# Optimization experiments

Hardware: AMD Instinct MI355X
Metric: run time of the kernel (lower is better)

## Reference

```python
import jax, jax.numpy as jnp
import numpy as np

B, L, D, H, HD, K = 1, 1024, 1024, 16, 64, 16
EPS = 1e-5

def _l2norm(x):
    n = jnp.sqrt(jnp.sum(x * x, axis=-1, keepdims=True))
    return x / jnp.maximum(n, 1e-12)

def _lin(x, w, b):
    return x @ w.T + b

def _lrelu2(x, alpha=0.01):
    y = jnp.where(x > 0, x, alpha * x)
    return y * y

def _forward(x, spectral_basis, M_phi_w, M_phi_b, wq_w, wq_b, wk_w, wk_b,
             wv_w, wv_b, wo_w, wo_b, wg_z_w, wg_z_b, kv_norm_scale):
    Bx, Lx, Dx = x.shape
    bhld = x.reshape(Bx, Lx, H, HD).transpose(0, 2, 1, 3)          # [B,H,L,h]
    # stu_conv: causal conv of every channel with each of K shared filters (FFT form)
    n = 2 * Lx
    Xf = jnp.fft.rfft(bhld, n=n, axis=2)                            # [B,H,F,h]
    Ff = jnp.fft.rfft(spectral_basis, n=n, axis=0)                  # [F,K]
    conv = jnp.fft.irfft(Xf[:, :, :, None, :] * Ff[None, None, :, :, None], n=n, axis=2)[:, :, :Lx]  # [B,H,L,K,h]
    x_tilde = conv.transpose(0, 2, 3, 1, 4).reshape(Bx, Lx, K * H * HD)
    x_tilde = _lin(x_tilde, M_phi_w, M_phi_b)                       # [B,L,D]
    q = _lin(x_tilde, wq_w, wq_b).reshape(Bx, Lx, H, HD).transpose(0, 2, 1, 3)
    k = _lin(x_tilde, wk_w, wk_b).reshape(Bx, Lx, H, HD).transpose(0, 2, 1, 3)
    v = _lin(x_tilde, wv_w, wv_b).reshape(Bx, Lx, H, HD).transpose(0, 2, 1, 3)
    k = _l2norm(k)
    v = _l2norm(v)
    sim = jnp.einsum('bhld,bhld->bhl', q, k)                        # [B,H,L]
    # Z[b,h,s,p,n] = k[b,h,s,n] * v[b,h,s,p]
    Z = v[..., :, None] * k[..., None, :]                           # [B,H,L,h,h]
    Z = Z * kv_norm_scale
    gates_logits = Z.reshape(Bx, H, Lx, HD * HD) @ wg_z_w.T + wg_z_b  # [B,H,L,1]
    gates_z = (_lrelu2(gates_logits) + EPS)[..., 0]                 # [B,H,L]
    gated_Z = Z * gates_z[..., None, None]
    # online-softmax associative scan over sequence: running (max, norm, exp-weighted v)
    def combine(a, b):
        ma, na, va = a
        mb, nb, vb = b
        m = jnp.maximum(ma, mb)
        ea = jnp.exp(ma - m)
        eb = jnp.exp(mb - m)
        return (m, na * ea + nb * eb, va * ea[..., None] + vb * eb[..., None])
    max_cumul, norm_cumul, v_cumul = jax.lax.associative_scan(
        combine, (sim, jnp.ones_like(sim), v), axis=2)
    Z_cumul = jnp.cumsum(gated_Z, axis=2)
    gate_cumul = jnp.cumsum(gates_z, axis=2)
    linear_attn = v_cumul / (norm_cumul[..., None] + EPS)           # [B,H,L,h]
    weights = jnp.exp(sim - max_cumul) / (norm_cumul + EPS)         # [B,H,L]
    Hm = Z_cumul / (gate_cumul[..., None, None] + EPS)              # [B,H,L,h,h]
    Y_base = jnp.einsum('bhtp,bhtpn->bhtn', q, Hm)                  # [B,H,L,h]
    # torch einsum broadcasts the size-1 p-dim of linear_attn.unsqueeze(-2):
    Y_lin = jnp.sum(q, axis=-1, keepdims=True) * linear_attn        # [B,H,L,h]
    Y = Y_base + (Y_lin - Y_base) * weights[..., None]
    Y = Y.transpose(0, 2, 1, 3).reshape(Bx, Lx, Dx)
    Y = _l2norm(Y)
    return _lin(Y, wo_w, wo_b)

def setup_inputs() -> dict:
    key = jax.random.key(0)
    ks = jax.random.split(key, 16)
    def nrm(k, shape, scale):
        return jax.random.normal(k, shape, dtype=jnp.float32) * scale
    return {
        'x': nrm(ks[0], (B, L, D), 1.0),
        'spectral_basis': nrm(ks[1], (L, K), 1.0 / np.sqrt(L)),
        'M_phi_w': nrm(ks[2], (D, K * H * HD), 1.0 / np.sqrt(K * H * HD)),
        'M_phi_b': jnp.zeros((D,), jnp.float32),
        'wq_w': nrm(ks[3], (D, D), 1.0 / np.sqrt(D)),
        'wq_b': jnp.zeros((D,), jnp.float32),
        'wk_w': nrm(ks[4], (D, D), 1.0 / np.sqrt(D)),
        'wk_b': jnp.zeros((D,), jnp.float32),
        'wv_w': nrm(ks[5], (D, D), 1.0 / np.sqrt(D)),
        'wv_b': jnp.zeros((D,), jnp.float32),
        'wo_w': nrm(ks[6], (D, D), 1.0 / np.sqrt(D)),
        'wo_b': jnp.zeros((D,), jnp.float32),
        'wg_z_w': nrm(ks[7], (1, HD * HD), 1.0 / np.sqrt(HD * HD)),
        'wg_z_b': jnp.zeros((1,), jnp.float32),
        'kv_norm_scale': jnp.ones((1, H, 1, 1, 1), jnp.float32),
    }

def reference(x, spectral_basis, M_phi_w, M_phi_b, wq_w, wq_b, wk_w, wk_b,
              wv_w, wv_b, wo_w, wo_b, wg_z_w, wg_z_b, kv_norm_scale):
    return _forward(x, spectral_basis, M_phi_w, M_phi_b, wq_w, wq_b, wk_w, wk_b,
                    wv_w, wv_b, wo_w, wo_b, wg_z_w, wg_z_b, kv_norm_scale)
```

## Files before the change

kernel.cpp:

```cpp
#include <hip/hip_runtime.h>
#include <hip/hip_bf16.h>

typedef __hip_bfloat16 bf16;
typedef __attribute__((ext_vector_type(8))) short short8;
typedef __attribute__((ext_vector_type(4))) float f32x4;

struct bf16x8 { bf16 v[8]; };
struct bf16x4 { bf16 v[4]; };

__device__ __forceinline__ void gload_lds16(const void* g, void* l) {
  __builtin_amdgcn_global_load_lds(
      (const __attribute__((address_space(1))) void*)g,
      (__attribute__((address_space(3))) void*)l, 16, 0, 0);
}

__device__ __forceinline__ float wave_sum(float x) {
#pragma unroll
  for (int o = 32; o > 0; o >>= 1) x += __shfl_xor(x, o, 64);
  return x;
}

__global__ void prep_cast_k(const float* __restrict__ mphiW,
                            const float* __restrict__ wq, const float* __restrict__ wk,
                            const float* __restrict__ wv, const float* __restrict__ wo,
                            const float* __restrict__ x,
                            const float* __restrict__ bq, const float* __restrict__ bk,
                            const float* __restrict__ bv,
                            bf16* __restrict__ mphi_bf, bf16* __restrict__ wqkv,
                            bf16* __restrict__ wo_bf, bf16* __restrict__ x_bf,
                            float* __restrict__ qkv_bias) {
  int b = blockIdx.x, tid = threadIdx.x;
  const float* src; bf16* dst; int i;
  if (b < 8192) { src = mphiW; dst = mphi_bf; i = b * 256 + tid; }
  else if (b < 10240) {
    int bb = b - 8192;
    src = (bb < 512) ? wq : (bb < 1024) ? wk : (bb < 1536) ? wv : wo;
    dst = (bb < 512) ? wqkv : (bb < 1024) ? (wqkv + 1048576)
         : (bb < 1536) ? (wqkv + 2097152) : wo_bf;
    i = (bb & 511) * 256 + tid;
  } else if (b < 10752) { src = x; dst = x_bf; i = (b - 10240) * 256 + tid; }
  else {
    int j = (b - 10752) * 256 + tid;
    if (j < 3072) {
      const float* s = (j < 1024) ? bq : (j < 2048) ? bk : bv;
      qkv_bias[j] = s[j & 1023];
    }
    return;
  }
  const float4* p = (const float4*)src + (size_t)i * 2;
  float4 a = p[0], c = p[1];
  bf16x8 o;
  o.v[0] = __float2bfloat16(a.x); o.v[1] = __float2bfloat16(a.y);
  o.v[2] = __float2bfloat16(a.z); o.v[3] = __float2bfloat16(a.w);
  o.v[4] = __float2bfloat16(c.x); o.v[5] = __float2bfloat16(c.y);
  o.v[6] = __float2bfloat16(c.z); o.v[7] = __float2bfloat16(c.w);
  ((bf16x8*)dst)[i] = o;
}

__global__ void build_T_k(const float* __restrict__ basis, bf16* __restrict__ T) {
  size_t i8 = (size_t)blockIdx.x * 256 + threadIdx.x;
  size_t i = i8 * 8;
  int s0 = (int)(i & 1023);
  int l = (int)((i >> 10) & 1023);
  int k = (int)(i >> 20);
  bf16x8 o;
#pragma unroll
  for (int j = 0; j < 8; j++) {
    int s = s0 + j;
    o.v[j] = (s <= l) ? __float2bfloat16(basis[(size_t)(l - s) * 16 + k])
                      : __float2bfloat16(0.f);
  }
  ((bf16x8*)T)[i8] = o;
}

template<int TRI, int OUTBF, int HASB, int DBUF>
__global__ void gemm_bt(const bf16* __restrict__ A, long sAb, int lda,
                        const bf16* __restrict__ B, long sBb, int ldb,
                        void* __restrict__ Cv, void* __restrict__ Cv2, int nbz1,
                        long sCb, int ldc,
                        const float* __restrict__ bias, int sbias, int K) {
  constexpr int NB = DBUF ? 2 : 1;
  __shared__ bf16 As[NB][128 * 64];
  __shared__ bf16 Bs[NB][128 * 64];
  const int tid = threadIdx.x;
  const int lane = tid & 63;
  const int wid = tid >> 6;
  const int wr = wid >> 1, wc = wid & 1;
  const int cpx = gridDim.x >> 3;
  const int logical = (blockIdx.x & 7) * cpx + (blockIdx.x >> 3);
  const int bx = logical & 7, by = (logical >> 3) & 7, bz = logical >> 6;
  const int r0 = by * 128, c0 = bx * 128;
  const bf16* Ab = A + (size_t)bz * sAb;
  const bf16* Bb = B + (size_t)bz * sBb;
  f32x4 acc[4][4] = {};
  const int nt = (TRI ? min(K, r0 + 128) : K) >> 6;

  const int srow = tid >> 3, scol = (tid & 7) << 3;

#define STAGE(buf, t)                                                         \
  {                                                                           \
    const int k0_ = (t) << 6;                                                 \
    _Pragma("unroll")                                                         \
    for (int i = 0; i < 4; i++) {                                             \
      int row = i * 32 + srow;                                                \
      gload_lds16(Ab + (size_t)(r0 + row) * lda + k0_ + scol,                 \
                  &As[buf][(row << 6) + scol]);                               \
    }                                                                         \
    _Pragma("unroll")                                                         \
    for (int i = 0; i < 4; i++) {                                             \
      int row = i * 32 + srow;                                                \
      gload_lds16(Bb + (size_t)(c0 + row) * ldb + k0_ + scol,                 \
                  &Bs[buf][(row << 6) + scol]);                               \
    }                                                                         \
  }

  int cur = 0;
  if (DBUF) STAGE(0, 0)
  for (int t = 0; t < nt; ++t) {
    if (DBUF) {
      if (t + 1 < nt) {
        STAGE(cur ^ 1, t + 1)
        asm volatile("s_waitcnt vmcnt(8)" ::: "memory");
      } else {
        asm volatile("s_waitcnt vmcnt(0)" ::: "memory");
      }
      __syncthreads();
    } else {
      __syncthreads();
      STAGE(0, t)
      asm volatile("s_waitcnt vmcnt(0)" ::: "memory");
      __syncthreads();
    }
#pragma unroll
    for (int ks = 0; ks < 2; ks++) {
      const int colo = ks * 32 + (lane >> 4) * 8;
      short8 af[4], bfr[4];
#pragma unroll
      for (int m = 0; m < 4; m++)
        af[m] = *(const short8*)&As[cur][(wr * 64 + m * 16 + (lane & 15)) * 64 + colo];
#pragma unroll
      for (int n = 0; n < 4; n++)
        bfr[n] = *(const short8*)&Bs[cur][(wc * 64 + n * 16 + (lane & 15)) * 64 + colo];
#pragma unroll
      for (int m = 0; m < 4; m++)
#pragma unroll
        for (int n = 0; n < 4; n++)
          acc[m][n] = __builtin_amdgcn_mfma_f32_16x16x32_bf16(af[m], bfr[n], acc[m][n], 0, 0, 0);
    }
    if (DBUF) { __syncthreads(); cur ^= 1; }
  }
#undef STAGE

  void* Cb = (bz < nbz1) ? Cv : Cv2;
  const int bzl = (bz < nbz1) ? bz : bz - nbz1;
  const int rb = r0 + wr * 64 + ((lane >> 4) << 2);
  const int cb = c0 + wc * 64 + (lane & 15);
#pragma unroll
  for (int n = 0; n < 4; n++) {
    const int col = cb + n * 16;
    float bv = HASB ? bias[bz * sbias + col] : 0.f;
#pragma unroll
    for (int m = 0; m < 4; m++) {
#pragma unroll
      for (int j = 0; j < 4; j++) {
        const int row = rb + m * 16 + j;
        size_t off = (size_t)bzl * sCb + (size_t)row * ldc + col;
        float v = acc[m][n][j] + bv;
        if (OUTBF) ((bf16*)Cb)[off] = __float2bfloat16(v);
        else       ((float*)Cb)[off] = v;
      }
    }
  }
}

__global__ void reduce16_k(const float* __restrict__ pA, const float* __restrict__ pB,
                           const float* __restrict__ bias, bf16* __restrict__ out) {
  int i4 = blockIdx.x * 256 + threadIdx.x;
  float4 v = *((const float4*)bias + (i4 & 255));
#pragma unroll
  for (int j = 0; j < 8; j++) {
    float4 a = *((const float4*)pA + i4 + j * 262144);
    v.x += a.x; v.y += a.y; v.z += a.z; v.w += a.w;
  }
#pragma unroll
  for (int j = 0; j < 8; j++) {
    float4 a = *((const float4*)pB + i4 + j * 262144);
    v.x += a.x; v.y += a.y; v.z += a.z; v.w += a.w;
  }
  bf16x4 o;
  o.v[0] = __float2bfloat16(v.x); o.v[1] = __float2bfloat16(v.y);
  o.v[2] = __float2bfloat16(v.z); o.v[3] = __float2bfloat16(v.w);
  ((bf16x4*)out)[i4] = o;
}

__global__ void reduce4f_k(const float* __restrict__ p, const float* __restrict__ bias,
                           float* __restrict__ out) {
  int i4 = blockIdx.x * 256 + threadIdx.x;
  float4 v = *((const float4*)bias + (i4 & 255));
#pragma unroll
  for (int j = 0; j < 4; j++) {
    float4 a = *((const float4*)p + i4 + j * 262144);
    v.x += a.x; v.y += a.y; v.z += a.z; v.w += a.w;
  }
  ((float4*)out)[i4] = v;
}

__global__ void qkv_post_k(const float* __restrict__ qkv, const float* __restrict__ W,
                           const float* __restrict__ wgb, const float* __restrict__ scale,
                           float* __restrict__ kn, float* __restrict__ vn,
                           float* __restrict__ sim, float* __restrict__ gz, float* __restrict__ qs) {
  __shared__ float Wl[64][65];
  int tid = threadIdx.x;
#pragma unroll
  for (int i = 0; i < 16; i++) {
    int c = i * 256 + tid;
    Wl[c >> 6][c & 63] = W[c];
  }
  __syncthreads();
  int lane = tid & 63;
  int gw = blockIdx.x * 4 + (tid >> 6);
  int h = gw >> 10, l = gw & 1023;
  const float* base = qkv + (size_t)l * 1024 + h * 64 + lane;
  float q = base[0];
  float k = base[1048576];
  float v = base[2097152];
  float knv = k * (1.f / fmaxf(sqrtf(wave_sum(k * k)), 1e-12f));
  float vnv = v * (1.f / fmaxf(sqrtf(wave_sum(v * v)), 1e-12f));
  float simv = wave_sum(q * knv);
  float qsv = wave_sum(q);
  float inner = 0.f;
#pragma unroll 8
  for (int n = 0; n < 64; n++)
    inner += Wl[lane][n] * __shfl(knv, n, 64);
  float gl = wave_sum(vnv * inner) * scale[h] + wgb[0];
  float yy = gl > 0.f ? gl : 0.01f * gl;
  float gzz = yy * yy + 1e-5f;
  size_t o = ((size_t)h * 1024 + l) * 64 + lane;
  kn[o] = knv; vn[o] = vnv;
  if (lane == 0) {
    sim[h * 1024 + l] = simv; gz[h * 1024 + l] = gzz; qs[h * 1024 + l] = qsv;
  }
}

__global__ void scan_outer_k(const float* __restrict__ sim, const float* __restrict__ gz,
                             const float* __restrict__ vn, const float* __restrict__ kn,
                             float* __restrict__ vloc, float* __restrict__ mloc,
                             float* __restrict__ nloc, float* __restrict__ gloc,
                             float* __restrict__ mA, float* __restrict__ nA,
                             float* __restrict__ vA, float* __restrict__ gA,
                             float* __restrict__ Mc) {
  __shared__ float vns[64][64], kns[64][64], gzs[64];
  int c = blockIdx.x, h = blockIdx.y, tid = threadIdx.x;
  size_t base = ((size_t)h * 1024 + c * 64) * 64;
#pragma unroll
  for (int i = 0; i < 16; i++) {
    int e = i * 256 + tid;
    vns[e >> 6][e & 63] = vn[base + e];
    kns[e >> 6][e & 63] = kn[base + e];
  }
  if (tid < 64) gzs[tid] = gz[h * 1024 + c * 64 + tid];
  __syncthreads();
  float acc[16] = {};
  for (int s = 0; s < 64; s++) {
    float g = gzs[s];
#pragma unroll
    for (int i = 0; i < 16; i++) {
      int pn = i * 256 + tid;
      acc[i] += (g * vns[s][pn >> 6]) * kns[s][pn & 63];
    }
  }
  size_t ob = (size_t)(h * 16 + c) * 4096;
#pragma unroll
  for (int i = 0; i < 16; i++) Mc[ob + i * 256 + tid] = acc[i];
  if (tid < 64) {
    int lane = tid;
    size_t hb = (size_t)h * 1024 + c * 64;
    float m = -1e30f, n = 0.f, v = 0.f, g = 0.f;
    for (int i = 0; i < 64; i++) {
      float s = sim[hb + i];
      float vv = vns[i][lane];
      float mn = fmaxf(m, s);
      float eo = expf(m - mn);
      float en = expf(s - mn);
      n = n * eo + en;
      v = v * eo + en * vv;
      m = mn;
      g += gzs[i];
      vloc[(hb + i) * 64 + lane] = v;
      if (lane == 0) { mloc[hb + i] = m; nloc[hb + i] = n; gloc[hb + i] = g; }
    }
    size_t ix = (size_t)h * 16 + c;
    vA[ix * 64 + lane] = v;
    if (lane == 0) { mA[ix] = m; nA[ix] = n; gA[ix] = g; }
  }
}

__global__ void chunk_prefix_k(const float* __restrict__ Mc, float* __restrict__ Sb) {
  int idx = blockIdx.x * 256 + threadIdx.x;
  int h = idx >> 12, pn = idx & 4095;
  float a = 0.f;
  for (int c = 0; c < 16; c++) {
    size_t o = (size_t)(h * 16 + c) * 4096 + pn;
    Sb[o] = a; a += Mc[o];
  }
}

__global__ void scan_apply_k(const float* __restrict__ sim,
                             const float* __restrict__ mloc, const float* __restrict__ nloc,
                             const float* __restrict__ gloc, const float* __restrict__ vloc,
                             const float* __restrict__ mA, const float* __restrict__ nA,
                             const float* __restrict__ gA, const float* __restrict__ vA,
                             float* __restrict__ linb, float* __restrict__ wtb,
                             float* __restrict__ gcb) {
  int c = blockIdx.x, h = blockIdx.y;
  int tid = threadIdx.x, lane = tid & 63, w = tid >> 6;
  float m = -1e30f, n = 0.f, v = 0.f, g = 0.f;
  for (int cc = 0; cc < c; cc++) {
    size_t ix = (size_t)h * 16 + cc;
    float mb = mA[ix], nb = nA[ix], gb = gA[ix];
    float vb = vA[ix * 64 + lane];
    float mn = fmaxf(m, mb);
    float ea = expf(m - mn), eb = expf(mb - mn);
    n = n * ea + nb * eb;
    v = v * ea + vb * eb;
    m = mn; g += gb;
  }
#pragma unroll 4
  for (int i = 0; i < 16; i++) {
    int row = w * 16 + i;
    int gw = h * 1024 + c * 64 + row;
    float ml = mloc[gw], nl = nloc[gw], gl = gloc[gw];
    float vl = vloc[(size_t)gw * 64 + lane];
    float mf = fmaxf(m, ml);
    float ep = expf(m - mf), el = expf(ml - mf);
    float nf = n * ep + nl * el;
    float vf = v * ep + vl * el;
    float inv = 1.f / (nf + 1e-5f);
    linb[(size_t)gw * 64 + lane] = vf * inv;
    if (lane == 0) {
      wtb[gw] = expf(sim[gw] - mf) * inv;
      gcb[gw] = g + gl;
    }
  }
}

__launch_bounds__(256)
__global__ void attn_mm_k(const float* __restrict__ qkvf, const float* __restrict__ vn,
                          const float* __restrict__ kn, const float* __restrict__ gz,
                          const float* __restrict__ qs, const float* __restrict__ Sb,
                          const float* __restrict__ wtb, const float* __restrict__ gcb,
                          const float* __restrict__ linb, const float* __restrict__ scale,
                          float* __restrict__ Yc) {
  __shared__ bf16 qs_[64 * 72], vs_[64 * 72], ksT[64 * 72], SsT[64 * 72], Ps[64 * 72];
  __shared__ float gzs[64];
  int c = blockIdx.x, h = blockIdx.y, tid = threadIdx.x;
  int lane = tid & 63, w = tid >> 6;
  size_t base = ((size_t)h * 1024 + c * 64) * 64;
#pragma unroll
  for (int i = 0; i < 16; i++) {
    int e = i * 256 + tid, r = e >> 6, cc = e & 63;
    qs_[r * 72 + cc] = __float2bfloat16(qkvf[(size_t)(c * 64 + r) * 1024 + h * 64 + cc]);
    vs_[r * 72 + cc] = __float2bfloat16(vn[base + e]);
    ksT[cc * 72 + r] = __float2bfloat16(kn[base + e]);
  }
  if (tid < 64) gzs[tid] = gz[h * 1024 + c * 64 + tid];
  {
    const float4* Sg = (const float4*)(Sb + ((size_t)h * 16 + c) * 4096);
#pragma unroll
    for (int j = 0; j < 4; j++) {
      int idx = tid * 4 + j;
      float4 f = Sg[idx];
      int p = idx >> 4, nb = (idx & 15) * 4;
      SsT[(nb + 0) * 72 + p] = __float2bfloat16(f.x);
      SsT[(nb + 1) * 72 + p] = __float2bfloat16(f.y);
      SsT[(nb + 2) * 72 + p] = __float2bfloat16(f.z);
      SsT[(nb + 3) * 72 + p] = __float2bfloat16(f.w);
    }
  }
  __syncthreads();
  const int fr = lane & 15, fq = lane >> 4;
  const int colo0 = fq * 8;
  {
    f32x4 pacc[4] = {};
#pragma unroll
    for (int ks2 = 0; ks2 < 2; ks2++) {
      int colo = ks2 * 32 + colo0;
      short8 a = *(const short8*)&qs_[(w * 16 + fr) * 72 + colo];
#pragma unroll
      for (int st = 0; st < 4; st++) {
        short8 b = *(const short8*)&vs_[(st * 16 + fr) * 72 + colo];
        pacc[st] = __builtin_amdgcn_mfma_f32_16x16x32_bf16(a, b, pacc[st], 0, 0, 0);
      }
    }
#pragma unroll
    for (int st = 0; st < 4; st++) {
      int s = st * 16 + fr;
      float g = gzs[s];
#pragma unroll
      for (int j = 0; j < 4; j++) {
        int t = w * 16 + fq * 4 + j;
        Ps[t * 72 + s] = __float2bfloat16((s <= t) ? pacc[st][j] * g : 0.f);
      }
    }
  }
  __syncthreads();
  f32x4 y[4] = {};
#pragma unroll
  for (int ks2 = 0; ks2 < 2; ks2++) {
    int colo = ks2 * 32 + colo0;
    short8 a  = *(const short8*)&qs_[(w * 16 + fr) * 72 + colo];
    short8 a2 = *(const short8*)&Ps[(w * 16 + fr) * 72 + colo];
#pragma unroll
    for (int nt = 0; nt < 4; nt++) {
      short8 b  = *(const short8*)&SsT[(nt * 16 + fr) * 72 + colo];
      short8 b2 = *(const short8*)&ksT[(nt * 16 + fr) * 72 + colo];
      y[nt] = __builtin_amdgcn_mfma_f32_16x16x32_bf16(a, b, y[nt], 0, 0, 0);
      y[nt] = __builtin_amdgcn_mfma_f32_16x16x32_bf16(a2, b2, y[nt], 0, 0, 0);
    }
  }
  float sc = scale[h];
#pragma unroll
  for (int j = 0; j < 4; j++) {
    int t = w * 16 + fq * 4 + j;
    int l = c * 64 + t;
    size_t il = (size_t)h * 1024 + l;
    float gcv = gcb[il], wv = wtb[il], qv = qs[il];
    float den = 1.f / (gcv + 1e-5f);
#pragma unroll
    for (int nt = 0; nt < 4; nt++) {
      int n = nt * 16 + fr;
      float yb = sc * y[nt][j] * den;
      float yl = qv * linb[il * 64 + n];
      Yc[(size_t)l * 1024 + h * 64 + n] = yb + (yl - yb) * wv;
    }
  }
}

__global__ void rownorm_cast_k(const float* __restrict__ Y, bf16* __restrict__ out) {
  __shared__ float red[4];
  int l = blockIdx.x, tid = threadIdx.x;
  float4 v = ((const float4*)(Y + (size_t)l * 1024))[tid];
  float ss = v.x * v.x + v.y * v.y + v.z * v.z + v.w * v.w;
  ss = wave_sum(ss);
  int wid = tid >> 6, lane = tid & 63;
  if (lane == 0) red[wid] = ss;
  __syncthreads();
  float tot = red[0] + red[1] + red[2] + red[3];
  float inv = 1.f / fmaxf(sqrtf(tot), 1e-12f);
  bf16x4 o;
  o.v[0] = __float2bfloat16(v.x * inv); o.v[1] = __float2bfloat16(v.y * inv);
  o.v[2] = __float2bfloat16(v.z * inv); o.v[3] = __float2bfloat16(v.w * inv);
  ((bf16x4*)(out + (size_t)l * 1024))[tid] = o;
}

extern "C" void kernel_launch(void* const* d_in, const int* in_sizes, int n_in,
                              void* d_out, int out_size, void* d_ws, size_t ws_size,
                              hipStream_t stream) {
  (void)in_sizes; (void)n_in; (void)out_size; (void)ws_size;
  const float* x     = (const float*)d_in[0];
  const float* basis = (const float*)d_in[1];
  const float* mphiW = (const float*)d_in[2];
  const float* mphiB = (const float*)d_in[3];
  const float* wqW = (const float*)d_in[4];  const float* wqB = (const float*)d_in[5];
  const float* wkW = (const float*)d_in[6];  const float* wkB = (const float*)d_in[7];
  const float* wvW = (const float*)d_in[8];  const float* wvB = (const float*)d_in[9];
  const float* woW = (const float*)d_in[10]; const float* woB = (const float*)d_in[11];
  const float* wgW = (const float*)d_in[12]; const float* wgB = (const float*)d_in[13];
  const float* kvs = (const float*)d_in[14];
  float* out = (float*)d_out;
  char* ws = (char*)d_ws;

  bf16*  Y_T     = (bf16*)(ws + 0x0000000UL);
  bf16*  Tbuf    = (bf16*)(ws + 0x2000000UL);
  bf16*  mphi_bf = (bf16*)(ws + 0x4000000UL);
  float* part2a  = (float*)(ws + 0x4000000UL);
  float* qkvf    = (float*)(ws + 0x4000000UL);
  float* part8   = (float*)(ws + 0x4000000UL);
  bf16*  x_bf    = (bf16*)(ws + 0x6000000UL);
  bf16*  xtil_bf = (bf16*)(ws + 0x6200000UL);
  bf16*  wqkv_bf = (bf16*)(ws + 0x6400000UL);
  bf16*  wo_bf   = (bf16*)(ws + 0x6A00000UL);
  float* qkv_bias= (float*)(ws + 0x6C00000UL);
  float* part2b  = (float*)(ws + 0x6C10000UL);
  float* kn      = (float*)(ws + 0x6C10000UL);
  float* vn      = (float*)(ws + 0x7010000UL);
  float* Mc      = (float*)(ws + 0x7410000UL);
  float* Yc      = (float*)(ws + 0x7810000UL);
  bf16*  ynorm   = (bf16*)(ws + 0x7C10000UL);
  float* simb    = (float*)(ws + 0x7E10000UL);
  float* gzb     = (float*)(ws + 0x7E20000UL);
  float* qsb     = (float*)(ws + 0x7E30000UL);
  float* wtb     = (float*)(ws + 0x7E40000UL);
  float* gcb     = (float*)(ws + 0x7E50000UL);
  float* vloc = (float*)(ws + 0x2000000UL);
  float* mloc = (float*)(ws + 0x2400000UL);
  float* nloc = (float*)(ws + 0x2410000UL);
  float* gloc = (float*)(ws + 0x2420000UL);
  float* mA   = (float*)(ws + 0x2430000UL);
  float* nA   = (float*)(ws + 0x2431000UL);
  float* gA   = (float*)(ws + 0x2432000UL);
  float* vA   = (float*)(ws + 0x2440000UL);
  float* linb = (float*)(ws + 0x2500000UL);
  float* Sb   = (float*)(ws + 0x2900000UL);

  prep_cast_k<<<10764, 256, 0, stream>>>(mphiW, wqW, wkW, wvW, woW, x, wqB, wkB, wvB,
                                         mphi_bf, wqkv_bf, wo_bf, x_bf, qkv_bias);
  build_T_k<<<8192, 256, 0, stream>>>(basis, Tbuf);

  gemm_bt<0, 1, 0, 0><<<1024, 256, 0, stream>>>(
      mphi_bf, 1024L, 16384, x_bf, 0L, 1024, (void*)Y_T, (void*)Y_T, 1 << 28,
      1048576L, 1024, nullptr, 0, 1024);

  gemm_bt<1, 0, 0, 0><<<1024, 256, 0, stream>>>(
      Tbuf, 1048576L, 1024, Y_T, 1048576L, 1024, (void*)part2a, (void*)part2b, 8,
      1048576L, 1024, nullptr, 0, 1024);
  reduce16_k<<<1024, 256, 0, stream>>>(part2a, part2b, mphiB, xtil_bf);

  gemm_bt<0, 0, 1, 1><<<192, 256, 0, stream>>>(
      xtil_bf, 0L, 1024, wqkv_bf, 1048576L, 1024, (void*)qkvf, (void*)qkvf, 1 << 28,
      1048576L, 1024, qkv_bias, 1024, 1024);

  qkv_post_k<<<4096, 256, 0, stream>>>(qkvf, wgW, wgB, kvs, kn, vn, simb, gzb, qsb);

  scan_outer_k<<<dim3(16, 16), 256, 0, stream>>>(simb, gzb, vn, kn,
                                                 vloc, mloc, nloc, gloc,
                                                 mA, nA, vA, gA, Mc);

  chunk_prefix_k<<<256, 256, 0, stream>>>(Mc, Sb);
  scan_apply_k<<<dim3(16, 16), 256, 0, stream>>>(simb, mloc, nloc, gloc, vloc,
                                                 mA, nA, gA, vA, linb, wtb, gcb);

  attn_mm_k<<<dim3(16, 16), 256, 0, stream>>>(qkvf, vn, kn, gzb, qsb, Sb,
                                              wtb, gcb, linb, kvs, Yc);

  rownorm_cast_k<<<1024, 256, 0, stream>>>(Yc, ynorm);

  gemm_bt<0, 0, 0, 1><<<256, 256, 0, stream>>>(
      ynorm, 256L, 1024, wo_bf, 256L, 1024, (void*)part8, (void*)part8, 1 << 28,
      1048576L, 1024, nullptr, 0, 256);
  reduce4f_k<<<1024, 256, 0, stream>>>(part8, woB, out);
}
```

Measured before the change: 242.6 us.

## Fuse T-build into prep, split-K the QKV GEMM, fold chunk prefix into attention

The Toeplitz-matrix build is merged into the cast kernel as extra blocks, which removes one launch. The QKV projection GEMM now splits K into two halves across 384 blocks instead of 192, which raises occupancy. The two partial sums and the bias are added at consumption time in qkv_post_k and attn_mm_k. The separate chunk-prefix kernel is dropped, and each attention block instead sums the preceding chunks' Mc directly. This trades a launch and a buffer for redundant reads that grow with chunk index.

```diff
diff --git a/kernel.cpp b/kernel.cpp
--- a/kernel.cpp
+++ b/kernel.cpp
@@ -26,10 +26,27 @@
                             const float* __restrict__ x,
                             const float* __restrict__ bq, const float* __restrict__ bk,
                             const float* __restrict__ bv,
+                            const float* __restrict__ basis,
                             bf16* __restrict__ mphi_bf, bf16* __restrict__ wqkv,
                             bf16* __restrict__ wo_bf, bf16* __restrict__ x_bf,
-                            float* __restrict__ qkv_bias) {
+                            float* __restrict__ qkv_bias, bf16* __restrict__ T) {
   int b = blockIdx.x, tid = threadIdx.x;
+  if (b >= 10764) {
+    size_t i8 = (size_t)(b - 10764) * 256 + tid;
+    size_t i = i8 * 8;
+    int s0 = (int)(i & 1023);
+    int l = (int)((i >> 10) & 1023);
+    int k = (int)(i >> 20);
+    bf16x8 o;
+#pragma unroll
+    for (int j = 0; j < 8; j++) {
+      int s = s0 + j;
+      o.v[j] = (s <= l) ? __float2bfloat16(basis[(size_t)(l - s) * 16 + k])
+                        : __float2bfloat16(0.f);
+    }
+    ((bf16x8*)T)[i8] = o;
+    return;
+  }
   const float* src; bf16* dst; int i;
   if (b < 8192) { src = mphiW; dst = mphi_bf; i = b * 256 + tid; }
   else if (b < 10240) {
@@ -57,23 +74,7 @@
   ((bf16x8*)dst)[i] = o;
 }
 
-__global__ void build_T_k(const float* __restrict__ basis, bf16* __restrict__ T) {
-  size_t i8 = (size_t)blockIdx.x * 256 + threadIdx.x;
-  size_t i = i8 * 8;
-  int s0 = (int)(i & 1023);
-  int l = (int)((i >> 10) & 1023);
-  int k = (int)(i >> 20);
-  bf16x8 o;
-#pragma unroll
-  for (int j = 0; j < 8; j++) {
-    int s = s0 + j;
-    o.v[j] = (s <= l) ? __float2bfloat16(basis[(size_t)(l - s) * 16 + k])
-                      : __float2bfloat16(0.f);
-  }
-  ((bf16x8*)T)[i8] = o;
-}
-
-template<int TRI, int OUTBF, int HASB, int DBUF>
+template<int TRI, int OUTBF, int HASB, int DBUF, int SK3>
 __global__ void gemm_bt(const bf16* __restrict__ A, long sAb, int lda,
                         const bf16* __restrict__ B, long sBb, int ldb,
                         void* __restrict__ Cv, void* __restrict__ Cv2, int nbz1,
@@ -90,8 +91,16 @@
   const int logical = (blockIdx.x & 7) * cpx + (blockIdx.x >> 3);
   const int bx = logical & 7, by = (logical >> 3) & 7, bz = logical >> 6;
   const int r0 = by * 128, c0 = bx * 128;
-  const bf16* Ab = A + (size_t)bz * sAb;
-  const bf16* Bb = B + (size_t)bz * sBb;
+  const bf16* Ab;
+  const bf16* Bb;
+  if (SK3) {
+    int w_ = bz % 3, kh_ = bz / 3;
+    Ab = A + kh_ * 512;
+    Bb = B + (size_t)w_ * sBb + kh_ * 512;
+  } else {
+    Ab = A + (size_t)bz * sAb;
+    Bb = B + (size_t)bz * sBb;
+  }
   f32x4 acc[4][4] = {};
   const int nt = (TRI ? min(K, r0 + 128) : K) >> 6;
 
@@ -207,6 +216,7 @@
 
 __global__ void qkv_post_k(const float* __restrict__ qkv, const float* __restrict__ W,
                            const float* __restrict__ wgb, const float* __restrict__ scale,
+                           const float* __restrict__ bias,
                            float* __restrict__ kn, float* __restrict__ vn,
                            float* __restrict__ sim, float* __restrict__ gz, float* __restrict__ qs) {
   __shared__ float Wl[64][65];
@@ -221,9 +231,9 @@
   int gw = blockIdx.x * 4 + (tid >> 6);
   int h = gw >> 10, l = gw & 1023;
   const float* base = qkv + (size_t)l * 1024 + h * 64 + lane;
-  float q = base[0];
-  float k = base[1048576];
-  float v = base[2097152];
+  float q = base[0] + base[3145728] + bias[h * 64 + lane];
+  float k = base[1048576] + base[4194304] + bias[1024 + h * 64 + lane];
+  float v = base[2097152] + base[5242880] + bias[2048 + h * 64 + lane];
   float knv = k * (1.f / fmaxf(sqrtf(wave_sum(k * k)), 1e-12f));
   float vnv = v * (1.f / fmaxf(sqrtf(wave_sum(v * v)), 1e-12f));
   float simv = wave_sum(q * knv);
@@ -292,16 +302,6 @@
     size_t ix = (size_t)h * 16 + c;
     vA[ix * 64 + lane] = v;
     if (lane == 0) { mA[ix] = m; nA[ix] = n; gA[ix] = g; }
-  }
-}
-
-__global__ void chunk_prefix_k(const float* __restrict__ Mc, float* __restrict__ Sb) {
-  int idx = blockIdx.x * 256 + threadIdx.x;
-  int h = idx >> 12, pn = idx & 4095;
-  float a = 0.f;
-  for (int c = 0; c < 16; c++) {
-    size_t o = (size_t)(h * 16 + c) * 4096 + pn;
-    Sb[o] = a; a += Mc[o];
   }
 }
 
@@ -347,10 +347,10 @@
 __launch_bounds__(256)
 __global__ void attn_mm_k(const float* __restrict__ qkvf, const float* __restrict__ vn,
                           const float* __restrict__ kn, const float* __restrict__ gz,
-                          const float* __restrict__ qs, const float* __restrict__ Sb,
+                          const float* __restrict__ qs, const float* __restrict__ Mc,
                           const float* __restrict__ wtb, const float* __restrict__ gcb,
                           const float* __restrict__ linb, const float* __restrict__ scale,
-                          float* __restrict__ Yc) {
+                          const float* __restrict__ bias, float* __restrict__ Yc) {
   __shared__ bf16 qs_[64 * 72], vs_[64 * 72], ksT[64 * 72], SsT[64 * 72], Ps[64 * 72];
   __shared__ float gzs[64];
   int c = blockIdx.x, h = blockIdx.y, tid = threadIdx.x;
@@ -359,22 +359,34 @@
 #pragma unroll
   for (int i = 0; i < 16; i++) {
     int e = i * 256 + tid, r = e >> 6, cc = e & 63;
-    qs_[r * 72 + cc] = __float2bfloat16(qkvf[(size_t)(c * 64 + r) * 1024 + h * 64 + cc]);
+    float qv = qkvf[(size_t)(c * 64 + r) * 1024 + h * 64 + cc]
+             + qkvf[(size_t)(c * 64 + r) * 1024 + h * 64 + cc + 3145728]
+             + bias[h * 64 + cc];
+    qs_[r * 72 + cc] = __float2bfloat16(qv);
     vs_[r * 72 + cc] = __float2bfloat16(vn[base + e]);
     ksT[cc * 72 + r] = __float2bfloat16(kn[base + e]);
   }
   if (tid < 64) gzs[tid] = gz[h * 1024 + c * 64 + tid];
   {
-    const float4* Sg = (const float4*)(Sb + ((size_t)h * 16 + c) * 4096);
+    float4 a0 = {0,0,0,0}, a1 = {0,0,0,0}, a2 = {0,0,0,0}, a3 = {0,0,0,0};
+    const float* McH = Mc + (size_t)h * 16 * 4096;
+    for (int cc = 0; cc < c; cc++) {
+      const float4* p = (const float4*)(McH + cc * 4096) + tid * 4;
+      float4 t0 = p[0], t1 = p[1], t2 = p[2], t3 = p[3];
+      a0.x += t0.x; a0.y += t0.y; a0.z += t0.z; a0.w += t0.w;
+      a1.x += t1.x; a1.y += t1.y; a1.z += t1.z; a1.w += t1.w;
+      a2.x += t2.x; a2.y += t2.y; a2.z += t2.z; a2.w += t2.w;
+      a3.x += t3.x; a3.y += t3.y; a3.z += t3.z; a3.w += t3.w;
+    }
+    float4 av[4] = {a0, a1, a2, a3};
 #pragma unroll
     for (int j = 0; j < 4; j++) {
       int idx = tid * 4 + j;
-      float4 f = Sg[idx];
       int p = idx >> 4, nb = (idx & 15) * 4;
-      SsT[(nb + 0) * 72 + p] = __float2bfloat16(f.x);
-      SsT[(nb + 1) * 72 + p] = __float2bfloat16(f.y);
-      SsT[(nb + 2) * 72 + p] = __float2bfloat16(f.z);
-      SsT[(nb + 3) * 72 + p] = __float2bfloat16(f.w);
+      SsT[(nb + 0) * 72 + p] = __float2bfloat16(av[j].x);
+      SsT[(nb + 1) * 72 + p] = __float2bfloat16(av[j].y);
+      SsT[(nb + 2) * 72 + p] = __float2bfloat16(av[j].z);
+      SsT[(nb + 3) * 72 + p] = __float2bfloat16(av[j].w);
     }
   }
   __syncthreads();
@@ -501,41 +513,40 @@
   float* gA   = (float*)(ws + 0x2432000UL);
   float* vA   = (float*)(ws + 0x2440000UL);
   float* linb = (float*)(ws + 0x2500000UL);
-  float* Sb   = (float*)(ws + 0x2900000UL);
-
-  prep_cast_k<<<10764, 256, 0, stream>>>(mphiW, wqW, wkW, wvW, woW, x, wqB, wkB, wvB,
-                                         mphi_bf, wqkv_bf, wo_bf, x_bf, qkv_bias);
-  build_T_k<<<8192, 256, 0, stream>>>(basis, Tbuf);
-
-  gemm_bt<0, 1, 0, 0><<<1024, 256, 0, stream>>>(
+
+  prep_cast_k<<<18956, 256, 0, stream>>>(mphiW, wqW, wkW, wvW, woW, x, wqB, wkB, wvB,
+                                         basis, mphi_bf, wqkv_bf, wo_bf, x_bf,
+                                         qkv_bias, Tbuf);
+
+  gemm_bt<0, 1, 0, 0, 0><<<1024, 256, 0, stream>>>(
       mphi_bf, 1024L, 16384, x_bf, 0L, 1024, (void*)Y_T, (void*)Y_T, 1 << 28,
       1048576L, 1024, nullptr, 0, 1024);
 
-  gemm_bt<1, 0, 0, 0><<<1024, 256, 0, stream>>>(
+  gemm_bt<1, 0, 0, 0, 0><<<1024, 256, 0, stream>>>(
       Tbuf, 1048576L, 1024, Y_T, 1048576L, 1024, (void*)part2a, (void*)part2b, 8,
       1048576L, 1024, nullptr, 0, 1024);
   reduce16_k<<<1024, 256, 0, stream>>>(part2a, part2b, mphiB, xtil_bf);
 
-  gemm_bt<0, 0, 1, 1><<<192, 256, 0, stream>>>(
+  gemm_bt<0, 0, 0, 1, 1><<<384, 256, 0, stream>>>(
       xtil_bf, 0L, 1024, wqkv_bf, 1048576L, 1024, (void*)qkvf, (void*)qkvf, 1 << 28,
-      1048576L, 1024, qkv_bias, 1024, 1024);
-
-  qkv_post_k<<<4096, 256, 0, stream>>>(qkvf, wgW, wgB, kvs, kn, vn, simb, gzb, qsb);
+      1048576L, 1024, nullptr, 0, 512);
+
+  qkv_post_k<<<4096, 256, 0, stream>>>(qkvf, wgW, wgB, kvs, qkv_bias,
+                                       kn, vn, simb, gzb, qsb);
 
   scan_outer_k<<<dim3(16, 16), 256, 0, stream>>>(simb, gzb, vn, kn,
                                                  vloc, mloc, nloc, gloc,
                                                  mA, nA, vA, gA, Mc);
 
-  chunk_prefix_k<<<256, 256, 0, stream>>>(Mc, Sb);
   scan_apply_k<<<dim3(16, 16), 256, 0, stream>>>(simb, mloc, nloc, gloc, vloc,
                                                  mA, nA, gA, vA, linb, wtb, gcb);
 
-  attn_mm_k<<<dim3(16, 16), 256, 0, stream>>>(qkvf, vn, kn, gzb, qsb, Sb,
-                                              wtb, gcb, linb, kvs, Yc);
+  attn_mm_k<<<dim3(16, 16), 256, 0, stream>>>(qkvf, vn, kn, gzb, qsb, Mc,
+                                              wtb, gcb, linb, kvs, qkv_bias, Yc);
 
   rownorm_cast_k<<<1024, 256, 0, stream>>>(Yc, ynorm);
 
-  gemm_bt<0, 0, 0, 1><<<256, 256, 0, stream>>>(
+  gemm_bt<0, 0, 0, 1, 0><<<256, 256, 0, stream>>>(
       ynorm, 256L, 1024, wo_bf, 256L, 1024, (void*)part8, (void*)part8, 1 << 28,
       1048576L, 1024, nullptr, 0, 256);
   reduce4f_k<<<1024, 256, 0, stream>>>(part8, woB, out);
```

Measured after the change: 234.1 us. 3.5% less time.
